# Optimization experiments

Hardware: AMD Instinct MI355X
Metric: run time of the kernel (lower is better)

## Reference

```python
import jax, jax.numpy as jnp
import numpy as np

B, T, D, H = 4096, 200, 64, 64


def setup_inputs() -> dict:
    key = jax.random.key(0)
    k1, k2, k3, k4, k5 = jax.random.split(key, 5)
    rnn_input = jax.random.normal(k1, (B, T, D), dtype=jnp.float32)
    sequence_length = jax.random.randint(k2, (B, 1), 0, T, dtype=jnp.int32)
    att_score = jax.random.uniform(k3, (B, T, 1), dtype=jnp.float32)
    s = 1.0 / np.sqrt(D + H)
    W_gate = jax.random.uniform(k4, (D + H, 2 * H), dtype=jnp.float32, minval=-s, maxval=s)
    b_gate = jnp.ones((2 * H,), dtype=jnp.float32)  # TF GRUCell gate bias init = 1.0
    W_cand = jax.random.uniform(k5, (D + H, H), dtype=jnp.float32, minval=-s, maxval=s)
    b_cand = jnp.zeros((H,), dtype=jnp.float32)
    return {"rnn_input": rnn_input, "sequence_length": sequence_length,
            "att_score": att_score, "W_gate": W_gate, "b_gate": b_gate,
            "W_cand": W_cand, "b_cand": b_cand}


def _augru_scan(x, att, seq_len, W_gate, b_gate, W_cand, b_cand):
    # x: [B,T,D], att: [B,T,1], seq_len: [B]
    Bx, Tx, _ = x.shape
    Hx = W_cand.shape[1]
    xs = jnp.swapaxes(x, 0, 1)          # [T,B,D]
    ats = jnp.swapaxes(att, 0, 1)       # [T,B,1]
    mask = (jnp.arange(Tx)[:, None] < seq_len[None, :])[..., None]  # [T,B,1]

    def step(h, inp):
        x_t, a_t, m_t = inp
        ru = jax.nn.sigmoid(jnp.concatenate([x_t, h], axis=-1) @ W_gate + b_gate)
        r, u = ru[:, :Hx], ru[:, Hx:]
        c = jnp.tanh(jnp.concatenate([x_t, r * h], axis=-1) @ W_cand + b_cand)
        u = (1.0 - a_t) * u                      # VecAttGRUCell (AUGRU) gate modulation
        new_h = u * h + (1.0 - u) * c            # TF GRUCell convention
        out = jnp.where(m_t, new_h, 0.0)         # dynamic_rnn zeros outputs past seq_len
        h_next = jnp.where(m_t, new_h, h)        # state copied through past seq_len
        return h_next, out

    h0 = jnp.zeros((Bx, Hx), dtype=x.dtype)
    h_final, outs = jax.lax.scan(step, h0, (xs, ats, mask))
    return jnp.swapaxes(outs, 0, 1), h_final     # [B,T,H], [B,H]


def reference(rnn_input, sequence_length, att_score, W_gate, b_gate, W_cand, b_cand):
    seq_len = jnp.squeeze(sequence_length, axis=-1)
    rnn_output, _ = _augru_scan(rnn_input, att_score, seq_len,
                                W_gate, b_gate, W_cand, b_cand)
    return rnn_output  # return_sequence=True
```

## Files before the change

kernel.cpp:

```cpp
#include <hip/hip_runtime.h>


typedef _Float16 half4_t __attribute__((ext_vector_type(4)));
typedef _Float16 half8_t __attribute__((ext_vector_type(8)));
typedef float    f32x4  __attribute__((ext_vector_type(4)));

#define T_MAX 200
#define H_DIM 64
#define M_TILE 16

__device__ __forceinline__ f32x4 mfma16(half8_t a, half8_t b, f32x4 c) {
    return __builtin_amdgcn_mfma_f32_16x16x32_f16(a, b, c, 0, 0, 0);
}
__device__ __forceinline__ int swz(int row, int byteInRow) {
    return (row * 128 + byteInRow) ^ ((row & 7) << 4);
}
__device__ __forceinline__ void lgkm_barrier() {
    asm volatile("s_waitcnt lgkmcnt(0)\n\ts_barrier" ::: "memory");
}

__global__ __launch_bounds__(256, 1) void augru_mfma(
    const float* __restrict__ X,
    const int*   __restrict__ SL,
    const float* __restrict__ ATT,
    const float* __restrict__ WG,
    const float* __restrict__ BG,
    const float* __restrict__ WC,
    const float* __restrict__ BC,
    float*       __restrict__ OUT)
{
    const int tid = threadIdx.x;
    const int w   = tid >> 6;
    const int l   = tid & 63;
    const int lr  = l & 15;
    const int lg  = l >> 4;
    const int b0  = blockIdx.x * M_TILE;

    __shared__ float    att_s[M_TILE][T_MAX];
    __shared__ int      sl_s[M_TILE];
    __shared__ _Float16 xb[2][16 * 64];
    __shared__ _Float16 hb[16 * 64];
    __shared__ _Float16 rhb[16 * 64];

#pragma unroll
    for (int k = 0; k < 4; ++k) {
        const int r = 4 * w + k;
        const float* ap = ATT + (size_t)(b0 + r) * T_MAX;
        for (int c = l; c < T_MAX; c += 64) att_s[r][c] = ap[c];
    }
    if (tid < M_TILE) {
        int v = SL[b0 + tid];
        sl_s[tid] = v < 0 ? 0 : (v > T_MAX ? T_MAX : v);
    }
    for (int i = tid; i < 16 * 64; i += 256) hb[i] = (_Float16)0.f;

    half8_t wgr[4], wgu[4], wcd[4];
    const int cr = 16 * w + lr;
    const int cu = 64 + cr;
#pragma unroll
    for (int kt = 0; kt < 4; ++kt) {
        const int kb = 32 * kt + 8 * lg;
        half8_t fr, fu, fc;
#pragma unroll
        for (int j = 0; j < 8; ++j) {
            fr[j] = (_Float16)WG[(size_t)(kb + j) * 128 + cr];
            fu[j] = (_Float16)WG[(size_t)(kb + j) * 128 + cu];
            fc[j] = (_Float16)WC[(size_t)(kb + j) * 64 + cr];
        }
        wgr[kt] = fr; wgu[kt] = fu; wcd[kt] = fc;
    }
    const float bias_r = BG[cr], bias_u = BG[cu], bias_c = BC[cr];

    const int xr = tid >> 4, xq = tid & 15;
    const float* xptr = X + (size_t)(b0 + xr) * (T_MAX * H_DIM) + 4 * xq;
    const int a_stg = swz(xr, 8 * xq);
    {
        float4 v0 = *(const float4*)(xptr);
        half4_t h4 = { (_Float16)v0.x, (_Float16)v0.y, (_Float16)v0.z, (_Float16)v0.w };
        *(half4_t*)((char*)xb[0] + a_stg) = h4;
    }
    float4 xv1 = *(const float4*)(xptr + 1 * H_DIM);

    __syncthreads();

    const int Lmax = max(
        max(max(sl_s[0], sl_s[1]), max(sl_s[2], sl_s[3])),
        max(max(max(sl_s[4], sl_s[5]), max(sl_s[6], sl_s[7])),
            max(max(sl_s[8], sl_s[9]), max(max(sl_s[10], sl_s[11]),
                max(max(sl_s[12], sl_s[13]), max(sl_s[14], sl_s[15]))))));
    int Lrow[4];
#pragma unroll
    for (int reg = 0; reg < 4; ++reg) Lrow[reg] = sl_s[4 * lg + reg];

    const int a_f0 = swz(lr, 16 * lg);
    const int a_f1 = swz(lr, 64 + 16 * lg);
    int a_c[4];
    size_t obase[4];
#pragma unroll
    for (int reg = 0; reg < 4; ++reg) {
        a_c[reg]   = swz(4 * lg + reg, 2 * cr);
        obase[reg] = (size_t)(b0 + 4 * lg + reg) * (T_MAX * H_DIM) + cr;
    }

    float hown[4] = {0.f, 0.f, 0.f, 0.f};

    for (int t = 0; t < Lmax; ++t) {
        const int pb = t & 1;
        int tn2 = t + 2; if (tn2 > T_MAX - 1) tn2 = T_MAX - 1;
        float4 xv2 = *(const float4*)(xptr + (size_t)tn2 * H_DIM);

        float attv[4];
#pragma unroll
        for (int reg = 0; reg < 4; ++reg) attv[reg] = att_s[4 * lg + reg][t];

        char* xbase = (char*)xb[pb];
        half8_t ax0 = *(half8_t*)(xbase + a_f0);
        half8_t ax1 = *(half8_t*)(xbase + a_f1);
        half8_t ah0 = *(half8_t*)((char*)hb + a_f0);
        half8_t ah1 = *(half8_t*)((char*)hb + a_f1);

        f32x4 accr = {bias_r, bias_r, bias_r, bias_r};
        f32x4 accu = {bias_u, bias_u, bias_u, bias_u};
        f32x4 accc = {bias_c, bias_c, bias_c, bias_c};
        accr = mfma16(ax0, wgr[0], accr);  accu = mfma16(ax0, wgu[0], accu);
        accc = mfma16(ax0, wcd[0], accc);
        accr = mfma16(ax1, wgr[1], accr);  accu = mfma16(ax1, wgu[1], accu);
        accc = mfma16(ax1, wcd[1], accc);
        accr = mfma16(ah0, wgr[2], accr);  accu = mfma16(ah0, wgu[2], accu);
        accr = mfma16(ah1, wgr[3], accr);  accu = mfma16(ah1, wgu[3], accu);

        float uu[4];
#pragma unroll
        for (int reg = 0; reg < 4; ++reg) {
            float rv = __fdividef(1.f, 1.f + __expf(-accr[reg]));
            *(_Float16*)((char*)rhb + a_c[reg]) = (_Float16)(rv * hown[reg]);
            uu[reg] = (1.f - attv[reg]) * __fdividef(1.f, 1.f + __expf(-accu[reg]));
        }
        lgkm_barrier();

        half8_t ar0 = *(half8_t*)((char*)rhb + a_f0);
        half8_t ar1 = *(half8_t*)((char*)rhb + a_f1);
        accc = mfma16(ar0, wcd[2], accc);
        accc = mfma16(ar1, wcd[3], accc);

#pragma unroll
        for (int reg = 0; reg < 4; ++reg) {
            float z  = accc[reg];
            float az = fabsf(z);
            float e2 = __expf(2.f * az);
            float c  = copysignf(1.f - __fdividef(2.f, e2 + 1.f), z);
            float hn = uu[reg] * hown[reg] + (1.f - uu[reg]) * c;
            bool  m  = (t < Lrow[reg]);
            OUT[obase[reg] + (size_t)t * H_DIM] = m ? hn : 0.f;
            if (m) hown[reg] = hn;
            *(_Float16*)((char*)hb + a_c[reg]) = (_Float16)hown[reg];
        }

        {
            half4_t h4 = { (_Float16)xv1.x, (_Float16)xv1.y, (_Float16)xv1.z, (_Float16)xv1.w };
            *(half4_t*)((char*)xb[pb ^ 1] + a_stg) = h4;
        }
        xv1 = xv2;
        lgkm_barrier();
    }

    {
        uint4 zz = make_uint4(0u, 0u, 0u, 0u);
        const int n4 = (T_MAX - Lmax) * (H_DIM / 4);
#pragma unroll
        for (int r = 0; r < M_TILE; ++r) {
            uint4* zp = (uint4*)(OUT + ((size_t)(b0 + r) * T_MAX + Lmax) * H_DIM);
            for (int i = tid; i < n4; i += 256) zp[i] = zz;
        }
    }
}

extern "C" void kernel_launch(void* const* d_in, const int* in_sizes, int n_in,
                              void* d_out, int out_size, void* d_ws, size_t ws_size,
                              hipStream_t stream) {
    const float* X   = (const float*)d_in[0];
    const int*   SL  = (const int*)d_in[1];
    const float* ATT = (const float*)d_in[2];
    const float* WG  = (const float*)d_in[3];
    const float* BG  = (const float*)d_in[4];
    const float* WC  = (const float*)d_in[5];
    const float* BC  = (const float*)d_in[6];
    float*       OUT = (float*)d_out;

    const int B = in_sizes[1];
    dim3 grid(B / M_TILE), block(256);
    augru_mfma<<<grid, block, 0, stream>>>(X, SL, ATT, WG, BG, WC, BC, OUT);
}
```

Before: 468.7 us.

## Give each wave its own four sequences to remove block barriers

```diff
diff --git a/kernel.cpp b/kernel.cpp
--- a/kernel.cpp
+++ b/kernel.cpp
@@ -7,19 +7,15 @@
 
 #define T_MAX 200
 #define H_DIM 64
-#define M_TILE 16
 
 __device__ __forceinline__ f32x4 mfma16(half8_t a, half8_t b, f32x4 c) {
     return __builtin_amdgcn_mfma_f32_16x16x32_f16(a, b, c, 0, 0, 0);
 }
-__device__ __forceinline__ int swz(int row, int byteInRow) {
-    return (row * 128 + byteInRow) ^ ((row & 7) << 4);
-}
-__device__ __forceinline__ void lgkm_barrier() {
-    asm volatile("s_waitcnt lgkmcnt(0)\n\ts_barrier" ::: "memory");
-}
-
-__global__ __launch_bounds__(256, 1) void augru_mfma(
+__device__ __forceinline__ float sigm(float x) {
+    return __fdividef(1.f, 1.f + __expf(-x));
+}
+
+__global__ __launch_bounds__(256, 1) void augru_wave(
     const float* __restrict__ X,
     const int*   __restrict__ SL,
     const float* __restrict__ ATT,
@@ -34,143 +30,154 @@
     const int l   = tid & 63;
     const int lr  = l & 15;
     const int lg  = l >> 4;
-    const int b0  = blockIdx.x * M_TILE;
-
-    __shared__ float    att_s[M_TILE][T_MAX];
-    __shared__ int      sl_s[M_TILE];
-    __shared__ _Float16 xb[2][16 * 64];
-    __shared__ _Float16 hb[16 * 64];
-    __shared__ _Float16 rhb[16 * 64];
-
-#pragma unroll
-    for (int k = 0; k < 4; ++k) {
-        const int r = 4 * w + k;
-        const float* ap = ATT + (size_t)(b0 + r) * T_MAX;
-        for (int c = l; c < T_MAX; c += 64) att_s[r][c] = ap[c];
-    }
-    if (tid < M_TILE) {
-        int v = SL[b0 + tid];
-        sl_s[tid] = v < 0 ? 0 : (v > T_MAX ? T_MAX : v);
-    }
-    for (int i = tid; i < 16 * 64; i += 256) hb[i] = (_Float16)0.f;
-
-    half8_t wgr[4], wgu[4], wcd[4];
-    const int cr = 16 * w + lr;
-    const int cu = 64 + cr;
-#pragma unroll
-    for (int kt = 0; kt < 4; ++kt) {
-        const int kb = 32 * kt + 8 * lg;
-        half8_t fr, fu, fc;
-#pragma unroll
-        for (int j = 0; j < 8; ++j) {
-            fr[j] = (_Float16)WG[(size_t)(kb + j) * 128 + cr];
-            fu[j] = (_Float16)WG[(size_t)(kb + j) * 128 + cu];
-            fc[j] = (_Float16)WC[(size_t)(kb + j) * 64 + cr];
-        }
-        wgr[kt] = fr; wgu[kt] = fu; wcd[kt] = fc;
-    }
-    const float bias_r = BG[cr], bias_u = BG[cu], bias_c = BC[cr];
-
-    const int xr = tid >> 4, xq = tid & 15;
-    const float* xptr = X + (size_t)(b0 + xr) * (T_MAX * H_DIM) + 4 * xq;
-    const int a_stg = swz(xr, 8 * xq);
+    const int sb  = blockIdx.x * 16 + 4 * w;
+
+    __shared__ __align__(16) _Float16 xb[4][2][5 * 64];
+    __shared__ __align__(16) _Float16 hb[4][5 * 64];
+    __shared__ __align__(16) _Float16 rhb[4][5 * 64];
+    __shared__ __align__(16) float    att_s[4][4][T_MAX];
+
+    for (int i = l; i < 5 * 64; i += 64) {
+        xb[w][0][i] = (_Float16)0.f; xb[w][1][i] = (_Float16)0.f;
+        hb[w][i]    = (_Float16)0.f; rhb[w][i]   = (_Float16)0.f;
+    }
+#pragma unroll
+    for (int s = 0; s < 4; ++s) {
+        const float* ap = ATT + (size_t)(sb + s) * T_MAX;
+        for (int c = l; c < T_MAX; c += 64) att_s[w][s][c] = ap[c];
+    }
+    int Ls[4]; int Lw = 0;
+#pragma unroll
+    for (int s = 0; s < 4; ++s) {
+        int v = SL[sb + s];
+        v = v < 0 ? 0 : (v > T_MAX ? T_MAX : v);
+        Ls[s] = v; Lw = max(Lw, v);
+    }
+
+    half8_t wg[8][4], wc[4][4];
+    float   bgv[8], bcv[4];
+#pragma unroll
+    for (int nt = 0; nt < 8; ++nt) {
+        const int col = 16 * nt + lr;
+#pragma unroll
+        for (int kt = 0; kt < 4; ++kt) {
+            const int kb = 32 * kt + 8 * lg;
+            half8_t f;
+#pragma unroll
+            for (int j = 0; j < 8; ++j) f[j] = (_Float16)WG[(size_t)(kb + j) * 128 + col];
+            wg[nt][kt] = f;
+        }
+        bgv[nt] = BG[col];
+    }
+#pragma unroll
+    for (int nt = 0; nt < 4; ++nt) {
+        const int col = 16 * nt + lr;
+#pragma unroll
+        for (int kt = 0; kt < 4; ++kt) {
+            const int kb = 32 * kt + 8 * lg;
+            half8_t f;
+#pragma unroll
+            for (int j = 0; j < 8; ++j) f[j] = (_Float16)WC[(size_t)(kb + j) * 64 + col];
+            wc[nt][kt] = f;
+        }
+        bcv[nt] = BC[col];
+    }
+
+    const int rowp = ((lr & 3) == 0) ? (lr >> 2) : 4;
+    const int off0 = rowp * 128 + ((16 * lg) ^ (rowp << 4));
+    const int off1 = rowp * 128 + ((64 + 16 * lg) ^ (rowp << 4));
+    int a_wr[4];
+#pragma unroll
+    for (int nt = 0; nt < 4; ++nt)
+        a_wr[nt] = lg * 128 + ((32 * nt + 2 * lr) ^ (lg << 4));
+    const int a_xs = lg * 128 + ((8 * lr) ^ (lg << 4));
+    const float* xsrc = X + (size_t)(sb + lg) * (T_MAX * H_DIM) + 4 * lr;
+
     {
-        float4 v0 = *(const float4*)(xptr);
+        float4 v0 = *(const float4*)xsrc;
         half4_t h4 = { (_Float16)v0.x, (_Float16)v0.y, (_Float16)v0.z, (_Float16)v0.w };
-        *(half4_t*)((char*)xb[0] + a_stg) = h4;
-    }
-    float4 xv1 = *(const float4*)(xptr + 1 * H_DIM);
-
-    __syncthreads();
-
-    const int Lmax = max(
-        max(max(sl_s[0], sl_s[1]), max(sl_s[2], sl_s[3])),
-        max(max(max(sl_s[4], sl_s[5]), max(sl_s[6], sl_s[7])),
-            max(max(sl_s[8], sl_s[9]), max(max(sl_s[10], sl_s[11]),
-                max(max(sl_s[12], sl_s[13]), max(sl_s[14], sl_s[15]))))));
-    int Lrow[4];
-#pragma unroll
-    for (int reg = 0; reg < 4; ++reg) Lrow[reg] = sl_s[4 * lg + reg];
-
-    const int a_f0 = swz(lr, 16 * lg);
-    const int a_f1 = swz(lr, 64 + 16 * lg);
-    int a_c[4];
-    size_t obase[4];
-#pragma unroll
-    for (int reg = 0; reg < 4; ++reg) {
-        a_c[reg]   = swz(4 * lg + reg, 2 * cr);
-        obase[reg] = (size_t)(b0 + 4 * lg + reg) * (T_MAX * H_DIM) + cr;
-    }
-
-    float hown[4] = {0.f, 0.f, 0.f, 0.f};
-
-    for (int t = 0; t < Lmax; ++t) {
-        const int pb = t & 1;
+        *(half4_t*)((char*)xb[w][0] + a_xs) = h4;
+    }
+    float4 xv1 = *(const float4*)(xsrc + H_DIM);
+
+    float  hown[4] = {0.f, 0.f, 0.f, 0.f};
+    const int   Lme   = Ls[lg];
+    const size_t obase = (size_t)(sb + lg) * (T_MAX * H_DIM) + lr;
+
+    for (int t = 0; t < Lw; ++t) {
+        const int cur = t & 1;
         int tn2 = t + 2; if (tn2 > T_MAX - 1) tn2 = T_MAX - 1;
-        float4 xv2 = *(const float4*)(xptr + (size_t)tn2 * H_DIM);
-
-        float attv[4];
-#pragma unroll
-        for (int reg = 0; reg < 4; ++reg) attv[reg] = att_s[4 * lg + reg][t];
-
-        char* xbase = (char*)xb[pb];
-        half8_t ax0 = *(half8_t*)(xbase + a_f0);
-        half8_t ax1 = *(half8_t*)(xbase + a_f1);
-        half8_t ah0 = *(half8_t*)((char*)hb + a_f0);
-        half8_t ah1 = *(half8_t*)((char*)hb + a_f1);
-
-        f32x4 accr = {bias_r, bias_r, bias_r, bias_r};
-        f32x4 accu = {bias_u, bias_u, bias_u, bias_u};
-        f32x4 accc = {bias_c, bias_c, bias_c, bias_c};
-        accr = mfma16(ax0, wgr[0], accr);  accu = mfma16(ax0, wgu[0], accu);
-        accc = mfma16(ax0, wcd[0], accc);
-        accr = mfma16(ax1, wgr[1], accr);  accu = mfma16(ax1, wgu[1], accu);
-        accc = mfma16(ax1, wcd[1], accc);
-        accr = mfma16(ah0, wgr[2], accr);  accu = mfma16(ah0, wgu[2], accu);
-        accr = mfma16(ah1, wgr[3], accr);  accu = mfma16(ah1, wgu[3], accu);
-
+        float4 xv2 = *(const float4*)(xsrc + (size_t)tn2 * H_DIM);
+
+        char* xB = (char*)xb[w][cur];
+        half8_t ax0 = *(half8_t*)(xB + off0);
+        half8_t ax1 = *(half8_t*)(xB + off1);
+        half8_t ah0 = *(half8_t*)((char*)hb[w] + off0);
+        half8_t ah1 = *(half8_t*)((char*)hb[w] + off1);
+
+        f32x4 g[8];
+#pragma unroll
+        for (int nt = 0; nt < 8; ++nt) {
+            f32x4 a = { bgv[nt], bgv[nt], bgv[nt], bgv[nt] };
+            a = mfma16(ax0, wg[nt][0], a);
+            a = mfma16(ax1, wg[nt][1], a);
+            a = mfma16(ah0, wg[nt][2], a);
+            a = mfma16(ah1, wg[nt][3], a);
+            g[nt] = a;
+        }
+        f32x4 cc[4];
+#pragma unroll
+        for (int nt = 0; nt < 4; ++nt) {
+            f32x4 a = { bcv[nt], bcv[nt], bcv[nt], bcv[nt] };
+            a = mfma16(ax0, wc[nt][0], a);
+            a = mfma16(ax1, wc[nt][1], a);
+            cc[nt] = a;
+        }
+
+        const float at = att_s[w][lg][t];
         float uu[4];
 #pragma unroll
-        for (int reg = 0; reg < 4; ++reg) {
-            float rv = __fdividef(1.f, 1.f + __expf(-accr[reg]));
-            *(_Float16*)((char*)rhb + a_c[reg]) = (_Float16)(rv * hown[reg]);
-            uu[reg] = (1.f - attv[reg]) * __fdividef(1.f, 1.f + __expf(-accu[reg]));
-        }
-        lgkm_barrier();
-
-        half8_t ar0 = *(half8_t*)((char*)rhb + a_f0);
-        half8_t ar1 = *(half8_t*)((char*)rhb + a_f1);
-        accc = mfma16(ar0, wcd[2], accc);
-        accc = mfma16(ar1, wcd[3], accc);
-
-#pragma unroll
-        for (int reg = 0; reg < 4; ++reg) {
-            float z  = accc[reg];
+        for (int nt = 0; nt < 4; ++nt) {
+            float rv = sigm(g[nt][0]);
+            *(_Float16*)((char*)rhb[w] + a_wr[nt]) = (_Float16)(rv * hown[nt]);
+            uu[nt] = (1.f - at) * sigm(g[4 + nt][0]);
+        }
+
+        half8_t ar0 = *(half8_t*)((char*)rhb[w] + off0);
+        half8_t ar1 = *(half8_t*)((char*)rhb[w] + off1);
+#pragma unroll
+        for (int nt = 0; nt < 4; ++nt) {
+            cc[nt] = mfma16(ar0, wc[nt][2], cc[nt]);
+            cc[nt] = mfma16(ar1, wc[nt][3], cc[nt]);
+        }
+
+#pragma unroll
+        for (int nt = 0; nt < 4; ++nt) {
+            float z  = cc[nt][0];
             float az = fabsf(z);
             float e2 = __expf(2.f * az);
             float c  = copysignf(1.f - __fdividef(2.f, e2 + 1.f), z);
-            float hn = uu[reg] * hown[reg] + (1.f - uu[reg]) * c;
-            bool  m  = (t < Lrow[reg]);
-            OUT[obase[reg] + (size_t)t * H_DIM] = m ? hn : 0.f;
-            if (m) hown[reg] = hn;
-            *(_Float16*)((char*)hb + a_c[reg]) = (_Float16)hown[reg];
+            float hn = uu[nt] * hown[nt] + (1.f - uu[nt]) * c;
+            bool  m  = (t < Lme);
+            OUT[obase + (size_t)t * H_DIM + 16 * nt] = m ? hn : 0.f;
+            if (m) hown[nt] = hn;
+            *(_Float16*)((char*)hb[w] + a_wr[nt]) = (_Float16)hown[nt];
         }
 
         {
             half4_t h4 = { (_Float16)xv1.x, (_Float16)xv1.y, (_Float16)xv1.z, (_Float16)xv1.w };
-            *(half4_t*)((char*)xb[pb ^ 1] + a_stg) = h4;
+            *(half4_t*)((char*)xb[w][cur ^ 1] + a_xs) = h4;
         }
         xv1 = xv2;
-        lgkm_barrier();
     }
 
     {
         uint4 zz = make_uint4(0u, 0u, 0u, 0u);
-        const int n4 = (T_MAX - Lmax) * (H_DIM / 4);
-#pragma unroll
-        for (int r = 0; r < M_TILE; ++r) {
-            uint4* zp = (uint4*)(OUT + ((size_t)(b0 + r) * T_MAX + Lmax) * H_DIM);
-            for (int i = tid; i < n4; i += 256) zp[i] = zz;
+        const int n4 = (T_MAX - Lw) * (H_DIM / 4);
+#pragma unroll
+        for (int s = 0; s < 4; ++s) {
+            uint4* zp = (uint4*)(OUT + ((size_t)(sb + s) * T_MAX + Lw) * H_DIM);
+            for (int i = l; i < n4; i += 64) zp[i] = zz;
         }
     }
 }
@@ -188,6 +195,6 @@
     float*       OUT = (float*)d_out;
 
     const int B = in_sizes[1];
-    dim3 grid(B / M_TILE), block(256);
-    augru_mfma<<<grid, block, 0, stream>>>(X, SL, ATT, WG, BG, WC, BC, OUT);
-}
+    dim3 grid(B / 16), block(256);
+    augru_wave<<<grid, block, 0, stream>>>(X, SL, ATT, WG, BG, WC, BC, OUT);
+}
```

After: 469.1 us. Within noise of the previous version (+0.1%).
